# Performance work log

Measured on AMD Instinct MI355X. Metric: run time of the kernel, lower is better.

Reference implementation:

```python
import jax, jax.numpy as jnp
import numpy as np

PC_MIN = jnp.array([0.0, -40.0, -3.0], dtype=jnp.float32)
VS_TOP = jnp.array([0.4, 0.4, 4.0], dtype=jnp.float32)
VS_MED = jnp.array([0.2, 0.2, 2.0], dtype=jnp.float32)
VS_LOW = jnp.array([0.1, 0.1, 1.0], dtype=jnp.float32)
GRID_TOP = (176, 200, 1)
GRID_MED = (352, 400, 2)
GRID_LOW = (704, 800, 4)
EPS = 1e-3
FILL = np.iinfo(np.int32).max


def _bn(x, g, b):
    # training-mode BatchNorm1d over the point/voxel axis (naiveSyncBN1d, eps=1e-3)
    mu = jnp.mean(x, axis=0)
    var = jnp.var(x, axis=0)
    return (x - mu) * jax.lax.rsqrt(var + EPS) * g + b


def _decode(lin, gx, gy, gz):
    x = lin % gx
    r = lin // gx
    y = r % gy
    r = r // gy
    z = r % gz
    b = r // gz
    return b, x, y, z


def _vfe(pts, batch, vs, grid, W1, g1, b1, W2, g2, b2):
    # Dynamic voxelization + DynamicScatterVFE (cluster center + voxel center, 2 layers, scatter-mean).
    N = pts.shape[0]
    gx, gy, gz = grid
    xyz = pts[:, :3]
    coors = jnp.floor((xyz - PC_MIN) / vs).astype(jnp.int32)
    cx = jnp.clip(coors[:, 0], 0, gx - 1)
    cy = jnp.clip(coors[:, 1], 0, gy - 1)
    cz = jnp.clip(coors[:, 2], 0, gz - 1)
    lin = ((batch * gz + cz) * gy + cy) * gx + cx  # linear voxel id incl. batch
    uniq, inv = jnp.unique(lin, return_inverse=True, size=N, fill_value=FILL)
    valid = uniq != FILL
    cnt = jnp.maximum(jax.ops.segment_sum(jnp.ones((N,), pts.dtype), inv, num_segments=N), 1.0)
    seg_mean = lambda v: jax.ops.segment_sum(v, inv, num_segments=N) / cnt[:, None]
    f_cluster = xyz - seg_mean(xyz)[inv]                      # offset from per-voxel point mean
    centers = PC_MIN + (jnp.stack([cx, cy, cz], axis=1).astype(pts.dtype) + 0.5) * vs
    f_center = xyz - centers                                   # offset from voxel center
    feats = jnp.concatenate([pts, f_cluster, f_center], axis=1)  # [N, 10]
    h = jax.nn.relu(_bn(feats @ W1, g1, b1))
    h = jnp.concatenate([h, seg_mean(h)[inv]], axis=1)           # point feat || gathered voxel feat
    h = jax.nn.relu(_bn(h @ W2, g2, b2))
    vox = seg_mean(h)
    return jnp.where(valid[:, None], vox, 0.0), uniq, valid


def _merge(sub_feats, sub_uniq, sub_valid, top_uniq, sub_grid, factor):
    # find_coordinate_indices + scatter_v2(mode='avg'): mean of child voxel feats per parent voxel.
    b, x, y, z = _decode(sub_uniq, *sub_grid)
    gx, gy, gz = GRID_TOP
    parent = ((b * gz + z // factor) * gy + y // factor) * gx + x // factor
    M = top_uniq.shape[0]
    pos = jnp.clip(jnp.searchsorted(top_uniq, parent), 0, M - 1)
    found = sub_valid & (top_uniq[pos] == parent)
    seg = jnp.where(found, pos, M)  # unmatched/padding rows dropped into slot M
    s = jax.ops.segment_sum(sub_feats, seg, num_segments=M + 1)[:M]
    c = jax.ops.segment_sum(found.astype(sub_feats.dtype), seg, num_segments=M + 1)[:M]
    return s / jnp.maximum(c, 1.0)[:, None]


def setup_inputs() -> dict:
    key = jax.random.key(0)
    ks = jax.random.split(key, 12)
    N, B = 262144, 2
    x = jax.random.uniform(ks[0], (N, 1), jnp.float32, 0.0, 70.4)
    y = jax.random.uniform(ks[1], (N, 1), jnp.float32, -40.0, 40.0)
    z = jax.random.uniform(ks[2], (N, 1), jnp.float32, -3.0, 1.0)
    inten = jax.random.uniform(ks[3], (N, 1), jnp.float32)
    bcol = jnp.repeat(jnp.arange(B, dtype=jnp.float32), N // B)[:, None]
    points = jnp.concatenate([bcol, x, y, z, inten], axis=1)
    lin_w = lambda k, i, o: jax.random.normal(k, (i, o), jnp.float32) * (1.0 / np.sqrt(i))
    return dict(
        points=points, batch_size=2,
        W1_top=lin_w(ks[4], 10, 64), g1_top=jnp.ones(64), b1_top=jnp.zeros(64),
        W2_top=lin_w(ks[5], 128, 128), g2_top=jnp.ones(128), b2_top=jnp.zeros(128),
        W1_med=lin_w(ks[6], 10, 32), g1_med=jnp.ones(32), b1_med=jnp.zeros(32),
        W2_med=lin_w(ks[7], 64, 64), g2_med=jnp.ones(64), b2_med=jnp.zeros(64),
        W1_low=lin_w(ks[8], 10, 32), g1_low=jnp.ones(32), b1_low=jnp.zeros(32),
        W2_low=lin_w(ks[9], 64, 64), g2_low=jnp.ones(64), b2_low=jnp.zeros(64),
    )


def reference(points, batch_size, W1_top, g1_top, b1_top, W2_top, g2_top, b2_top,
              W1_med, g1_med, b1_med, W2_med, g2_med, b2_med,
              W1_low, g1_low, b1_low, W2_low, g2_low, b2_low):
    batch = points[:, 0].astype(jnp.int32)
    pts = points[:, 1:]
    vf, top_uniq, top_valid = _vfe(pts, batch, VS_TOP, GRID_TOP, W1_top, g1_top, b1_top, W2_top, g2_top, b2_top)
    mfeat, med_uniq, med_valid = _vfe(pts, batch, VS_MED, GRID_MED, W1_med, g1_med, b1_med, W2_med, g2_med, b2_med)
    lfeat, low_uniq, low_valid = _vfe(pts, batch, VS_LOW, GRID_LOW, W1_low, g1_low, b1_low, W2_low, g2_low, b2_low)
    med_mean = _merge(mfeat, med_uniq, med_valid, top_uniq, GRID_MED, 2)
    low_mean = _merge(lfeat, low_uniq, low_valid, top_uniq, GRID_LOW, 4)
    merged = jnp.where(top_valid[:, None], jnp.concatenate([med_mean, low_mean], axis=1), 0.0)
    b, x, y, z = _decode(top_uniq, *GRID_TOP)
    coors = jnp.where(top_valid[:, None], jnp.stack([b, z, y, x], axis=1), -1)
    return vf, merged, coors
```

## Files before the change

kernel.cpp:

```cpp
#include <hip/hip_runtime.h>
#include <cstdint>
#include <cstddef>

#define NPTS 262144
#define BLK 256
#define TGX 176
#define TGY 200
#define TGZ 1

#define G_TOPC 70400
#define G_MEDC 1126400
#define G_LOWC 4505600

#define SCAN_ITEMS 32
#define SCAN_CHUNK (BLK*SCAN_ITEMS)
#define NB_T 9
#define NB_M 138
#define NB_L 550
#define BO_T 0
#define BO_M 16
#define BO_L 160
#define NBVT (G_TOPC/BLK)
#define NBVM (NPTS/BLK)
#define NBVL (NPTS/BLK)

#define Y2B (NPTS/128)
#define ST1BLKS 256
#define NHT 4400
#define NHM 8192
#define NJT 8800
#define NJM 16384
#define NCL 275

struct SP {
  const float4* srt; const int* jr; const float4* vm;
  const float* W1; const float* W2;
  const float* g1; const float* b1; const float* g2; const float* b2;
  const int* cnt; const int* uniq; const int* woff; const int* U;
  float* segt; float* part1; float* part2;
  float* coef1; float* coef2;
  unsigned short* Y2;
  float* hout;
  int C1; int segstride; int gx, gy, gz; float vx, vy, vz;
};

__device__ __forceinline__ unsigned short f2bf(float v) {
  unsigned u = __float_as_uint(v);
  u += 0x7FFFu + ((u >> 16) & 1u);
  return (unsigned short)(u >> 16);
}
__device__ __forceinline__ float bf2f(unsigned short h) {
  return __uint_as_float((unsigned)h << 16);
}

__device__ __forceinline__ void pcoords(float x, float y, float z,
    float vx, float vy, float vz, int gx, int gy, int gz,
    int& cx, int& cy, int& cz) {
  cx = (int)floorf((x - 0.0f)  / vx);
  cy = (int)floorf((y + 40.0f) / vy);
  cz = (int)floorf((z + 3.0f)  / vz);
  cx = min(max(cx, 0), gx - 1);
  cy = min(max(cy, 0), gy - 1);
  cz = min(max(cz, 0), gz - 1);
}

__device__ __forceinline__ int lin3(float b, float x, float y, float z,
    float vx, float vy, float vz, int gx, int gy, int gz) {
  int cx, cy, cz; pcoords(x, y, z, vx, vy, vz, gx, gy, gz, cx, cy, cz);
  return (((int)b * gz + cz) * gy + cy) * gx + cx;
}

__device__ __forceinline__ void build_f(float4 p, float4 vm,
    float vx, float vy, float vz, int gx, int gy, int gz, float* f) {
  int cx, cy, cz; pcoords(p.x, p.y, p.z, vx, vy, vz, gx, gy, gz, cx, cy, cz);
  f[0] = p.x; f[1] = p.y; f[2] = p.z; f[3] = p.w;
  f[4] = p.x - vm.x;
  f[5] = p.y - vm.y;
  f[6] = p.z - vm.z;
  f[7] = p.x - (0.0f   + (cx + 0.5f)*vx);
  f[8] = p.y - (-40.0f + (cy + 0.5f)*vy);
  f[9] = p.z - (-3.0f  + (cz + 0.5f)*vz);
}

__global__ __launch_bounds__(BLK) void k_count3(const float* __restrict__ pts,
    int* __restrict__ ct, int* __restrict__ cm, int* __restrict__ cl) {
  int i = blockIdx.x * BLK + threadIdx.x;
  if (i >= NPTS) return;
  float b = pts[i*5+0], x = pts[i*5+1], y = pts[i*5+2], z = pts[i*5+3];
  atomicAdd(&ct[lin3(b,x,y,z, 0.4f,0.4f,4.0f, 176,200,1)], 1);
  atomicAdd(&cm[lin3(b,x,y,z, 0.2f,0.2f,2.0f, 352,400,2)], 1);
  atomicAdd(&cl[lin3(b,x,y,z, 0.1f,0.1f,1.0f, 704,800,4)], 1);
}

__global__ __launch_bounds__(BLK) void k_scan1_all(const int* __restrict__ ct,
    const int* __restrict__ cm, const int* __restrict__ cl,
    int2* __restrict__ bsum) {
  int bid = blockIdx.x;
  const int* cnt; int G, bo, cb;
  if (bid < NB_T)            { cnt = ct; G = G_TOPC; bo = BO_T; cb = bid; }
  else if (bid < NB_T+NB_M)  { cnt = cm; G = G_MEDC; bo = BO_M; cb = bid - NB_T; }
  else                       { cnt = cl; G = G_LOWC; bo = BO_L; cb = bid - NB_T - NB_M; }
  int base = cb * SCAN_CHUNK + threadIdx.x * SCAN_ITEMS;
  int so = 0, sp = 0;
  #pragma unroll
  for (int k = 0; k < SCAN_ITEMS; k++) {
    int j = base + k;
    if (j < G) { int c = cnt[j]; if (c > 0) { so++; sp += c; } }
  }
  __shared__ int sho[BLK], shp[BLK];
  sho[threadIdx.x] = so; shp[threadIdx.x] = sp; __syncthreads();
  for (int off = BLK/2; off > 0; off >>= 1) {
    if (threadIdx.x < off) {
      sho[threadIdx.x] += sho[threadIdx.x + off];
      shp[threadIdx.x] += shp[threadIdx.x + off];
    }
    __syncthreads();
  }
  if (threadIdx.x == 0) { int2 v; v.x = sho[0]; v.y = shp[0]; bsum[bo + cb] = v; }
}

__device__ void scan_pass(int2* bsum, int off, int nb, int* U,
                          int* so, int* sp) {
  int t = threadIdx.x;
  int vo = 0, vp = 0;
  if (t < nb) { int2 v = bsum[off + t]; vo = v.x; vp = v.y; }
  so[t] = vo; sp[t] = vp; __syncthreads();
  for (int o = 1; o < 1024; o <<= 1) {
    int ao = (t >= o) ? so[t - o] : 0;
    int ap = (t >= o) ? sp[t - o] : 0;
    __syncthreads();
    so[t] += ao; sp[t] += ap;
    __syncthreads();
  }
  if (t < nb) { int2 e; e.x = so[t] - vo; e.y = sp[t] - vp; bsum[off + t] = e; }
  if (t == 0) *U = so[1023];
  __syncthreads();
}

__global__ __launch_bounds__(1024) void k_scan2_all(int2* __restrict__ bsum,
    int* __restrict__ Ut, int* __restrict__ Um, int* __restrict__ Ul) {
  __shared__ int so[1024], sp[1024];
  scan_pass(bsum, BO_T, NB_T, Ut, so, sp);
  scan_pass(bsum, BO_M, NB_M, Um, so, sp);
  scan_pass(bsum, BO_L, NB_L, Ul, so, sp);
}

__global__ __launch_bounds__(BLK) void k_scan3_all(const int* __restrict__ ct,
    const int* __restrict__ cm, const int* __restrict__ cl,
    const int2* __restrict__ bsum,
    int* __restrict__ rkt, int* __restrict__ rkm, int* __restrict__ rkl,
    int* __restrict__ uqt, int* __restrict__ uqm, int* __restrict__ uql,
    int* __restrict__ wot, int* __restrict__ wom, int* __restrict__ wol) {
  int bid = blockIdx.x;
  const int* cnt; int G, bo, cb; int *rank, *uniq, *woff;
  if (bid < NB_T)           { cnt=ct; G=G_TOPC; bo=BO_T; cb=bid;            rank=rkt; uniq=uqt; woff=wot; }
  else if (bid < NB_T+NB_M) { cnt=cm; G=G_MEDC; bo=BO_M; cb=bid-NB_T;       rank=rkm; uniq=uqm; woff=wom; }
  else                      { cnt=cl; G=G_LOWC; bo=BO_L; cb=bid-NB_T-NB_M;  rank=rkl; uniq=uql; woff=wol; }
  int base = cb * SCAN_CHUNK + threadIdx.x * SCAN_ITEMS;
  int so = 0, sp = 0;
  #pragma unroll
  for (int k = 0; k < SCAN_ITEMS; k++) {
    int j = base + k;
    if (j < G) { int c = cnt[j]; if (c > 0) { so++; sp += c; } }
  }
  __shared__ int sho[BLK], shp[BLK];
  sho[threadIdx.x] = so; shp[threadIdx.x] = sp; __syncthreads();
  for (int off = 1; off < BLK; off <<= 1) {
    int ao = (threadIdx.x >= off) ? sho[threadIdx.x - off] : 0;
    int ap = (threadIdx.x >= off) ? shp[threadIdx.x - off] : 0;
    __syncthreads();
    sho[threadIdx.x] += ao; shp[threadIdx.x] += ap;
    __syncthreads();
  }
  int2 bb = bsum[bo + cb];
  int ro = bb.x + sho[threadIdx.x] - so;
  int po = bb.y + shp[threadIdx.x] - sp;
  for (int k = 0; k < SCAN_ITEMS; k++) {
    int j = base + k;
    if (j < G) {
      int c = cnt[j];
      if (c > 0) { rank[j] = ro; uniq[ro] = j; woff[ro] = po; ro++; po += c; }
    }
  }
}

__global__ __launch_bounds__(BLK) void k_scatter3(const float* __restrict__ pts,
    const int* __restrict__ rkt, int* __restrict__ wot, float4* __restrict__ st, int* __restrict__ jt,
    const int* __restrict__ rkm, int* __restrict__ wom, float4* __restrict__ sm, int* __restrict__ jm,
    const int* __restrict__ rkl, int* __restrict__ wol, float4* __restrict__ sl, int* __restrict__ jl) {
  int i = blockIdx.x * BLK + threadIdx.x;
  if (i >= NPTS) return;
  float b = pts[i*5+0], x = pts[i*5+1], y = pts[i*5+2], z = pts[i*5+3], it = pts[i*5+4];
  float4 p; p.x = x; p.y = y; p.z = z; p.w = it;
  {
    int r = rkt[lin3(b,x,y,z, 0.4f,0.4f,4.0f, 176,200,1)];
    int j = atomicAdd(&wot[r], 1); st[j] = p; jt[j] = r;
  }
  {
    int r = rkm[lin3(b,x,y,z, 0.2f,0.2f,2.0f, 352,400,2)];
    int j = atomicAdd(&wom[r], 1); sm[j] = p; jm[j] = r;
  }
  {
    int r = rkl[lin3(b,x,y,z, 0.1f,0.1f,1.0f, 704,800,4)];
    int j = atomicAdd(&wol[r], 1); sl[j] = p; jl[j] = r;
  }
}

__global__ __launch_bounds__(BLK) void k_vox13(
    const float4* __restrict__ st, const int* __restrict__ uqt, const int* __restrict__ ct,
    const int* __restrict__ wot, const int* __restrict__ Ut, float4* __restrict__ vt,
    const float4* __restrict__ sm, const int* __restrict__ uqm, const int* __restrict__ cm,
    const int* __restrict__ wom, const int* __restrict__ Um, float4* __restrict__ vm,
    const float4* __restrict__ sl, const int* __restrict__ uql, const int* __restrict__ cl,
    const int* __restrict__ wol, const int* __restrict__ Ul, float4* __restrict__ vl) {
  int bid = blockIdx.x;
  const float4* srt; const int *uniq, *cnt, *woff, *Up; float4* vmean; int r;
  if (bid < NBVT)           { r = bid*BLK + threadIdx.x;           srt=st; uniq=uqt; cnt=ct; woff=wot; Up=Ut; vmean=vt; }
  else if (bid < NBVT+NBVM) { r = (bid-NBVT)*BLK + threadIdx.x;    srt=sm; uniq=uqm; cnt=cm; woff=wom; Up=Um; vmean=vm; }
  else                      { r = (bid-NBVT-NBVM)*BLK + threadIdx.x; srt=sl; uniq=uql; cnt=cl; woff=wol; Up=Ul; vmean=vl; }
  if (r >= *Up) return;
  int lin = uniq[r];
  int len = cnt[lin];
  int base = woff[r] - len;
  float sx = 0.f, sy = 0.f, sz = 0.f;
  for (int k = 0; k < len; k++) {
    float4 p = srt[base + k];
    sx += p.x; sy += p.y; sz += p.z;
  }
  float il = 1.0f / (float)len;
  float4 o; o.x = sx*il; o.y = sy*il; o.z = sz*il; o.w = il;
  vmean[r] = o;
}

__global__ __launch_bounds__(BLK) void k_stats1_all(SP a, SP b, SP c) {
  int s = blockIdx.x >> 8;
  int blk = blockIdx.x & 255;
  SP sp = (s == 0) ? a : ((s == 1) ? b : c);
  const int C1 = sp.C1;
  __shared__ float w[640];
  __shared__ float wsum[4][64], wsq[4][64];
  for (int t = threadIdx.x; t < 10*C1; t += BLK) w[t] = sp.W1[t];
  __syncthreads();
  float f[4][10];
  #pragma unroll
  for (int k = 0; k < 4; k++) {
    int i = blk*1024 + k*BLK + threadIdx.x;
    float4 p = sp.srt[i];
    float4 vmn = sp.vm[sp.jr[i]];
    build_f(p, vmn, sp.vx, sp.vy, sp.vz, sp.gx, sp.gy, sp.gz, f[k]);
  }
  int wv = threadIdx.x >> 6;
  int lane = threadIdx.x & 63;
  for (int o = 0; o < C1; o += 4) {
    float sacc[4] = {0,0,0,0}, qacc[4] = {0,0,0,0};
    #pragma unroll
    for (int k = 0; k < 4; k++) {
      float a0=0.f, a1=0.f, a2=0.f, a3=0.f;
      #pragma unroll
      for (int d = 0; d < 10; d++) {
        float fv = f[k][d];
        const float* wr = &w[d*C1 + o];
        a0 = fmaf(fv, wr[0], a0); a1 = fmaf(fv, wr[1], a1);
        a2 = fmaf(fv, wr[2], a2); a3 = fmaf(fv, wr[3], a3);
      }
      sacc[0] += a0; sacc[1] += a1; sacc[2] += a2; sacc[3] += a3;
      qacc[0] += a0*a0; qacc[1] += a1*a1; qacc[2] += a2*a2; qacc[3] += a3*a3;
    }
    #pragma unroll
    for (int m = 1; m < 64; m <<= 1) {
      #pragma unroll
      for (int e = 0; e < 4; e++) {
        sacc[e] += __shfl_xor(sacc[e], m);
        qacc[e] += __shfl_xor(qacc[e], m);
      }
    }
    if (lane == 0) {
      #pragma unroll
      for (int e = 0; e < 4; e++) { wsum[wv][o+e] = sacc[e]; wsq[wv][o+e] = qacc[e]; }
    }
  }
  __syncthreads();
  if (threadIdx.x < C1) {
    int ch = threadIdx.x;
    float sv = wsum[0][ch] + wsum[1][ch] + wsum[2][ch] + wsum[3][ch];
    float qv = wsq[0][ch] + wsq[1][ch] + wsq[2][ch] + wsq[3][ch];
    sp.part1[(size_t)blk*2*C1 + ch]      = sv;
    sp.part1[(size_t)blk*2*C1 + C1 + ch] = qv;
  }
}

__device__ __forceinline__ void partcoef_body(const float* part, int NB, int C,
    int ch, const float* g, const float* b, float* coef) {
  float s = 0.f, q = 0.f;
  for (int bk = threadIdx.x; bk < NB; bk += BLK) {
    s += part[(size_t)bk*2*C + ch];
    q += part[(size_t)bk*2*C + C + ch];
  }
  __shared__ float ss[BLK], sq[BLK];
  ss[threadIdx.x] = s; sq[threadIdx.x] = q; __syncthreads();
  for (int off = BLK/2; off > 0; off >>= 1) {
    if (threadIdx.x < off) {
      ss[threadIdx.x] += ss[threadIdx.x + off];
      sq[threadIdx.x] += sq[threadIdx.x + off];
    }
    __syncthreads();
  }
  if (threadIdx.x == 0) {
    float mu  = ss[0] * (1.0f / NPTS);
    float var = sq[0] * (1.0f / NPTS) - mu*mu;
    float sc  = g[ch] * (1.0f / sqrtf(var + 1e-3f));
    coef[ch]     = sc;
    coef[C + ch] = fmaf(-mu, sc, b[ch]);
  }
}

__global__ __launch_bounds__(BLK) void k_partcoef1_all(SP a, SP b, SP c) {
  int bid = blockIdx.x; SP sp; int ch;
  if (bid < 64)      { sp = a; ch = bid; }
  else if (bid < 96) { sp = b; ch = bid - 64; }
  else               { sp = c; ch = bid - 96; }
  if (ch >= sp.C1) return;
  partcoef_body(sp.part1, ST1BLKS, sp.C1, ch, sp.g1, sp.b1, sp.coef1);
}

__global__ __launch_bounds__(BLK) void k_partcoef2_all(SP a, SP b, SP c) {
  int bid = blockIdx.x; SP sp; int ch;
  if (bid < 128)      { sp = a; ch = bid; }
  else if (bid < 192) { sp = b; ch = bid - 128; }
  else                { sp = c; ch = bid - 192; }
  if (ch >= 2*sp.C1) return;
  partcoef_body(sp.part2, Y2B, 2*sp.C1, ch, sp.g2, sp.b2, sp.coef2);
}

__global__ __launch_bounds__(BLK) void k_hsegT_all(SP a, SP b, SP c) {
  int bid = blockIdx.x; SP sp; int rb;
  if (bid < NHT)           { sp = a; rb = bid; }
  else if (bid < NHT+NHM)  { sp = b; rb = bid - NHT; }
  else                     { sp = c; rb = bid - NHT - NHM; }
  const int C1 = sp.C1;
  const int qsh = (C1 == 64) ? 4 : 3;
  __shared__ float w[640];
  __shared__ float sc[64], sb[64];
  for (int t = threadIdx.x; t < 10*C1; t += BLK) w[t] = sp.W1[t];
  for (int t = threadIdx.x; t < C1; t += BLK) { sc[t] = sp.coef1[t]; sb[t] = sp.coef1[C1 + t]; }
  __syncthreads();
  int tid = rb * BLK + threadIdx.x;
  int r = tid >> qsh;
  int q = tid & ((1 << qsh) - 1);
  if (r >= *sp.U) return;
  int lin = sp.uniq[r];
  int len = sp.cnt[lin];
  int base = sp.woff[r] - len;
  float4 vmn = sp.vm[r];
  int c0 = q * 4;
  float s0 = sc[c0+0], s1 = sc[c0+1], s2 = sc[c0+2], s3 = sc[c0+3];
  float o0 = sb[c0+0], o1 = sb[c0+1], o2 = sb[c0+2], o3 = sb[c0+3];
  float a0=0.f, a1=0.f, a2=0.f, a3=0.f;
  for (int k = 0; k < len; k++) {
    float4 p = sp.srt[base + k];
    float f[10];
    build_f(p, vmn, sp.vx, sp.vy, sp.vz, sp.gx, sp.gy, sp.gz, f);
    float y0=0.f, y1=0.f, y2=0.f, y3=0.f;
    #pragma unroll
    for (int d = 0; d < 10; d++) {
      float fv = f[d];
      const float* wr = &w[d*C1 + c0];
      y0 = fmaf(fv, wr[0], y0); y1 = fmaf(fv, wr[1], y1);
      y2 = fmaf(fv, wr[2], y2); y3 = fmaf(fv, wr[3], y3);
    }
    a0 += fmaxf(fmaf(y0, s0, o0), 0.f);
    a1 += fmaxf(fmaf(y1, s1, o1), 0.f);
    a2 += fmaxf(fmaf(y2, s2, o2), 0.f);
    a3 += fmaxf(fmaf(y3, s3, o3), 0.f);
  }
  float il = 1.0f / (float)len;
  sp.segt[(size_t)(c0+0)*sp.segstride + r] = a0*il;
  sp.segt[(size_t)(c0+1)*sp.segstride + r] = a1*il;
  sp.segt[(size_t)(c0+2)*sp.segstride + r] = a2*il;
  sp.segt[(size_t)(c0+3)*sp.segstride + r] = a3*il;
}

#define FMA4(ACC, AV, BV) { (ACC).x = fmaf((AV), (BV).x, (ACC).x); \
  (ACC).y = fmaf((AV), (BV).y, (ACC).y); \
  (ACC).z = fmaf((AV), (BV).z, (ACC).z); \
  (ACC).w = fmaf((AV), (BV).w, (ACC).w); }

template<int C1>
__device__ __forceinline__ void y2t_body(const SP& sp, int blk,
    float* At, float* Bp) {
  constexpr int C2  = 2*C1;
  constexpr int K   = 2*C1;
  constexpr int MT  = 128;
  constexpr int KC  = 32;
  constexpr int NKC = K / KC;
  constexpr int NP  = C2 / 64;
  const int tid  = threadIdx.x;
  const int base = blk * MT;

  const int jst = tid & 127;
  const int qst = tid >> 7;
  int    jr_s = sp.jr[base + jst];
  float4 p_s  = sp.srt[base + jst];
  float4 vm_s = sp.vm[jr_s];
  float fs[10];
  build_f(p_s, vm_s, sp.vx, sp.vy, sp.vz, sp.gx, sp.gy, sp.gz, fs);

  const int w      = tid >> 6;
  const int lane   = tid & 63;
  const int colg   = lane & 15;
  const int rowsub = lane >> 4;
  const int rowg   = w*4 + rowsub;
  const int arow   = rowg*8;

  float4 acc[NP][8];
  #pragma unroll
  for (int p = 0; p < NP; p++)
    #pragma unroll
    for (int rr = 0; rr < 8; rr++) acc[p][rr] = {0.f, 0.f, 0.f, 0.f};

  #pragma unroll
  for (int kc = 0; kc < NKC; kc++) {
    if (kc) __syncthreads();
    if (kc*KC < C1) {
      #pragma unroll
      for (int m = 0; m < 4; m++) {
        int qq = qst + 2*m;
        int c0 = kc*KC + qq*4;
        float y0=0.f, y1=0.f, y2=0.f, y3=0.f;
        #pragma unroll
        for (int d = 0; d < 10; d++) {
          float fv = fs[d];
          const float* wr = &sp.W1[d*C1 + c0];
          y0 = fmaf(fv, wr[0], y0); y1 = fmaf(fv, wr[1], y1);
          y2 = fmaf(fv, wr[2], y2); y3 = fmaf(fv, wr[3], y3);
        }
        At[(qq*4+0)*MT + jst] = fmaxf(fmaf(y0, sp.coef1[c0+0], sp.coef1[C1+c0+0]), 0.f);
        At[(qq*4+1)*MT + jst] = fmaxf(fmaf(y1, sp.coef1[c0+1], sp.coef1[C1+c0+1]), 0.f);
        At[(qq*4+2)*MT + jst] = fmaxf(fmaf(y2, sp.coef1[c0+2], sp.coef1[C1+c0+2]), 0.f);
        At[(qq*4+3)*MT + jst] = fmaxf(fmaf(y3, sp.coef1[c0+3], sp.coef1[C1+c0+3]), 0.f);
      }
    } else {
      #pragma unroll
      for (int m = 0; m < 16; m++) {
        int k = qst + 2*m;
        int segch = kc*KC + k - C1;
        At[k*MT + jst] = sp.segt[(size_t)segch*sp.segstride + jr_s];
      }
    }
    constexpr int BQ = KC*C2/4;
    for (int it = tid; it < BQ; it += BLK) {
      int k  = it / (C2/4);
      int c4 = it % (C2/4);
      *(float4*)&Bp[k*C2 + c4*4] =
          *(const float4*)&sp.W2[(size_t)(kc*KC + k)*C2 + c4*4];
    }
    __syncthreads();
    #pragma unroll 8
    for (int k = 0; k < KC; k++) {
      float4 a0 = *(const float4*)&At[k*MT + arow];
      float4 a1 = *(const float4*)&At[k*MT + arow + 4];
      #pragma unroll
      for (int p = 0; p < NP; p++) {
        float4 bv = *(const float4*)&Bp[k*C2 + p*64 + colg*4];
        FMA4(acc[p][0], a0.x, bv); FMA4(acc[p][1], a0.y, bv);
        FMA4(acc[p][2], a0.z, bv); FMA4(acc[p][3], a0.w, bv);
        FMA4(acc[p][4], a1.x, bv); FMA4(acc[p][5], a1.y, bv);
        FMA4(acc[p][6], a1.z, bv); FMA4(acc[p][7], a1.w, bv);
      }
    }
  }

  #pragma unroll
  for (int p = 0; p < NP; p++)
    #pragma unroll
    for (int rr = 0; rr < 8; rr++) {
      float4 v = acc[p][rr];
      ushort4 h; h.x = f2bf(v.x); h.y = f2bf(v.y); h.z = f2bf(v.z); h.w = f2bf(v.w);
      *(ushort4*)&sp.Y2[(size_t)(base + arow + rr)*C2 + p*64 + colg*4] = h;
    }

  __syncthreads();
  float* red = At;
  #pragma unroll
  for (int p = 0; p < NP; p++) {
    #pragma unroll
    for (int e = 0; e < 4; e++) {
      float sv = 0.f, qv = 0.f;
      #pragma unroll
      for (int rr = 0; rr < 8; rr++) {
        float v = (&acc[p][rr].x)[e];
        sv += v; qv += v*v;
      }
      red[rowg*C2 + p*64 + colg*4 + e]        = sv;
      red[(16 + rowg)*C2 + p*64 + colg*4 + e] = qv;
    }
  }
  __syncthreads();
  if (tid < C2) {
    float sv = 0.f, qv = 0.f;
    #pragma unroll 4
    for (int i = 0; i < 16; i++) {
      sv += red[i*C2 + tid];
      qv += red[(16 + i)*C2 + tid];
    }
    sp.part2[(size_t)blk*2*C2 + tid]      = sv;
    sp.part2[(size_t)blk*2*C2 + C2 + tid] = qv;
  }
}

__global__ __launch_bounds__(BLK) void k_y2t_all(SP a, SP b, SP c) {
  __shared__ float At[32*128];
  __shared__ float Bp[32*128];
  int bid = blockIdx.x;
  if (bid < Y2B)        y2t_body<64>(a, bid, At, Bp);
  else if (bid < 2*Y2B) y2t_body<32>(b, bid - Y2B, At, Bp);
  else                  y2t_body<32>(c, bid - 2*Y2B, At, Bp);
}

__global__ __launch_bounds__(BLK) void k_hseg2_all(SP a, SP b, SP c) {
  int bid = blockIdx.x; SP sp; int rb;
  if (bid < NJT)           { sp = a; rb = bid; }
  else if (bid < NJT+NJM)  { sp = b; rb = bid - NJT; }
  else                     { sp = c; rb = bid - NJT - NJM; }
  const int C = 2*sp.C1;
  const int qsh = (C == 128) ? 5 : 4;
  __shared__ float sc[128], sb[128];
  for (int t = threadIdx.x; t < C; t += BLK) { sc[t] = sp.coef2[t]; sb[t] = sp.coef2[C + t]; }
  __syncthreads();
  int tid = rb * BLK + threadIdx.x;
  int r = tid >> qsh;
  int q = tid & ((1 << qsh) - 1);
  if (r >= *sp.U) return;
  int lin = sp.uniq[r];
  int len = sp.cnt[lin];
  int base = sp.woff[r] - len;
  int c0 = q * 4;
  float s0 = sc[c0+0], s1 = sc[c0+1], s2 = sc[c0+2], s3 = sc[c0+3];
  float o0 = sb[c0+0], o1 = sb[c0+1], o2 = sb[c0+2], o3 = sb[c0+3];
  float a0=0.f, a1=0.f, a2=0.f, a3=0.f;
  const unsigned short* Yh = sp.Y2;
  for (int k = 0; k < len; k++) {
    ushort4 hv = *(const ushort4*)&Yh[(size_t)(base + k)*C + c0];
    a0 += fmaxf(fmaf(bf2f(hv.x), s0, o0), 0.f);
    a1 += fmaxf(fmaf(bf2f(hv.y), s1, o1), 0.f);
    a2 += fmaxf(fmaf(bf2f(hv.z), s2, o2), 0.f);
    a3 += fmaxf(fmaf(bf2f(hv.w), s3, o3), 0.f);
  }
  float il = 1.0f / (float)len;
  float4 o = {a0*il, a1*il, a2*il, a3*il};
  *(float4*)&sp.hout[(size_t)r*C + c0] = o;
}

__global__ __launch_bounds__(BLK) void k_clist_all(const int* __restrict__ tuniq,
    const int* __restrict__ Utp,
    const int* __restrict__ cnt_m, const int* __restrict__ rank_m,
    int* __restrict__ clist_m, int* __restrict__ mcnt_m,
    const int* __restrict__ cnt_l, const int* __restrict__ rank_l,
    int* __restrict__ clist_l, int* __restrict__ mcnt_l) {
  int bid = blockIdx.x;
  const int *scnt, *srank; int *clist, *mcnt;
  int gx, gy, gz, f, rb;
  if (bid < NCL) { scnt=cnt_m; srank=rank_m; clist=clist_m; mcnt=mcnt_m;
                   gx=352; gy=400; gz=2; f=2; rb=bid; }
  else           { scnt=cnt_l; srank=rank_l; clist=clist_l; mcnt=mcnt_l;
                   gx=704; gy=800; gz=4; f=4; rb=bid-NCL; }
  int r = rb * BLK + threadIdx.x;
  if (r >= *Utp) return;
  int lin = tuniq[r];
  int x = lin % TGX; int t = lin / TGX;
  int y = t % TGY;   int b = t / TGY;
  int m = 0;
  for (int cz = 0; cz < gz; cz++)
    for (int yy = y*f; yy < y*f + f; yy++)
      for (int xx = x*f; xx < x*f + f; xx++) {
        int cl = ((b*gz + cz)*gy + yy)*gx + xx;
        if (scnt[cl] > 0) clist[(size_t)r*64 + (m++)] = srank[cl];
      }
  mcnt[r] = m;
}

__global__ __launch_bounds__(BLK) void k_merge2_all(
    const float* __restrict__ vox_m, const int* __restrict__ clist_m,
    const int* __restrict__ mcnt_m, float* __restrict__ maccm,
    const float* __restrict__ vox_l, const int* __restrict__ clist_l,
    const int* __restrict__ mcnt_l, float* __restrict__ maccl,
    const int* __restrict__ Utp) {
  int bid = blockIdx.x;
  const float* vox; const int *clist, *mcnt; float* dest; int rb;
  if (bid < NHT) { vox=vox_m; clist=clist_m; mcnt=mcnt_m; dest=maccm; rb=bid; }
  else           { vox=vox_l; clist=clist_l; mcnt=mcnt_l; dest=maccl; rb=bid-NHT; }
  int idx = rb * BLK + threadIdx.x;
  int r = idx >> 4;
  int q = idx & 15;
  if (r >= *Utp) return;
  int m = mcnt[r];
  float a0=0.f, a1=0.f, a2=0.f, a3=0.f;
  for (int t = 0; t < m; t++) {
    int cr = clist[(size_t)r*64 + t];
    float4 v = *(const float4*)&vox[(size_t)cr*64 + q*4];
    a0 += v.x; a1 += v.y; a2 += v.z; a3 += v.w;
  }
  float inv = 1.0f / (float)max(m, 1);
  float4 o = {a0*inv, a1*inv, a2*inv, a3*inv};
  *(float4*)&dest[(size_t)r*64 + q*4] = o;
}

__global__ __launch_bounds__(BLK) void k_fin_all(const int* __restrict__ uniq,
    const int* __restrict__ Up, const float* __restrict__ maccm,
    const float* __restrict__ maccl, float* __restrict__ vf,
    float* __restrict__ mg, float* __restrict__ coors) {
  int idx = blockIdx.x * BLK + threadIdx.x;
  int r = idx >> 5;
  int q = idx & 31;
  if (r >= NPTS) return;
  int U = *Up;
  float4 v = {0.f, 0.f, 0.f, 0.f};
  if (r < U)
    v = (q < 16) ? *(const float4*)&maccm[(size_t)r*64 + q*4]
                 : *(const float4*)&maccl[(size_t)r*64 + (q-16)*4];
  *(float4*)&mg[(size_t)r*128 + q*4] = v;
  if (r >= U) {
    float4 z = {0.f, 0.f, 0.f, 0.f};
    *(float4*)&vf[(size_t)r*128 + q*4] = z;
  }
  if (q == 0) {
    float4 co;
    if (r < U) {
      int lin = uniq[r];
      int x = lin % TGX; int t = lin / TGX;
      int y = t % TGY;   t /= TGY;
      int z = t % TGZ;   int b = t / TGZ;
      co.x = (float)b; co.y = (float)z; co.z = (float)y; co.w = (float)x;
    } else {
      co.x = -1.f; co.y = -1.f; co.z = -1.f; co.w = -1.f;
    }
    *(float4*)&coors[(size_t)r*4] = co;
  }
}

extern "C" void kernel_launch(void* const* d_in, const int* in_sizes, int n_in,
                              void* d_out, int out_size, void* d_ws, size_t ws_size,
                              hipStream_t stream) {
  const float* pts = (const float*)d_in[0];

  float* out = (float*)d_out;
  float* vf = out;
  float* mg = out + (size_t)NPTS * 128;
  float* co = out + (size_t)NPTS * 256;

  char* w = (char*)d_ws;
  size_t off = 0;
  auto alloc = [&](size_t bytes) -> void* {
    void* p = w + off;
    off = (off + bytes + 1023) & ~(size_t)1023;
    return p;
  };
  int*    cnt_t   = (int*)alloc(((size_t)G_TOPC + G_MEDC + G_LOWC) * 4);
  int*    cnt_m   = cnt_t + G_TOPC;
  int*    cnt_l   = cnt_t + G_TOPC + G_MEDC;
  int*    rank_t  = (int*)alloc((size_t)G_TOPC * 4);
  int*    rank_m  = (int*)alloc((size_t)G_MEDC * 4);
  int*    rank_l  = (int*)alloc((size_t)G_LOWC * 4);
  int*    uniq_t  = (int*)alloc((size_t)G_TOPC * 4);
  int*    uniq_m  = (int*)alloc((size_t)NPTS * 4);
  int*    uniq_l  = (int*)alloc((size_t)NPTS * 4);
  int*    woff_t  = (int*)alloc((size_t)G_TOPC * 4);
  int*    woff_m  = (int*)alloc((size_t)NPTS * 4);
  int*    woff_l  = (int*)alloc((size_t)NPTS * 4);
  float4* srt_t   = (float4*)alloc((size_t)NPTS * 16);
  float4* srt_m   = (float4*)alloc((size_t)NPTS * 16);
  float4* srt_l   = (float4*)alloc((size_t)NPTS * 16);
  int*    jr_t    = (int*)alloc((size_t)NPTS * 4);
  int*    jr_m    = (int*)alloc((size_t)NPTS * 4);
  int*    jr_l    = (int*)alloc((size_t)NPTS * 4);
  float4* vm_t    = (float4*)alloc((size_t)G_TOPC * 16);
  float4* vm_m    = (float4*)alloc((size_t)NPTS * 16);
  float4* vm_l    = (float4*)alloc((size_t)NPTS * 16);
  float*  segt_t  = (float*)alloc((size_t)G_TOPC * 64 * 4);
  float*  segt_m  = (float*)alloc((size_t)NPTS * 32 * 4);
  float*  segt_l  = (float*)alloc((size_t)NPTS * 32 * 4);
  float*  vox_m   = (float*)alloc((size_t)NPTS * 64 * 4);
  float*  vox_l   = (float*)alloc((size_t)NPTS * 64 * 4);
  unsigned short* Y2h_t = (unsigned short*)alloc((size_t)NPTS * 128 * 2);
  unsigned short* Y2h_m = (unsigned short*)alloc((size_t)NPTS * 64 * 2);
  unsigned short* Y2h_l = (unsigned short*)alloc((size_t)NPTS * 64 * 2);
  int*    clist_m = (int*)alloc((size_t)G_TOPC * 64 * 4);
  int*    clist_l = (int*)alloc((size_t)G_TOPC * 64 * 4);
  int*    mcnt_m  = (int*)alloc((size_t)G_TOPC * 4);
  int*    mcnt_l  = (int*)alloc((size_t)G_TOPC * 4);
  float*  maccm   = (float*)alloc((size_t)G_TOPC * 64 * 4);
  float*  maccl   = (float*)alloc((size_t)G_TOPC * 64 * 4);
  float*  part1_t = (float*)alloc((size_t)ST1BLKS * 128 * 4);
  float*  part1_m = (float*)alloc((size_t)ST1BLKS * 64 * 4);
  float*  part1_l = (float*)alloc((size_t)ST1BLKS * 64 * 4);
  float*  part2_t = (float*)alloc((size_t)Y2B * 256 * 4);
  float*  part2_m = (float*)alloc((size_t)Y2B * 128 * 4);
  float*  part2_l = (float*)alloc((size_t)Y2B * 128 * 4);
  float*  coef    = (float*)alloc(6 * 256 * 4);
  int2*   bsum    = (int2*)alloc(1024 * 8);
  int*    Ut      = (int*)alloc(64);
  int*    Um      = (int*)alloc(64);
  int*    Ul      = (int*)alloc(64);
  (void)in_sizes; (void)n_in; (void)out_size; (void)ws_size;

  auto mkSP = [&](int scaleIdx) -> SP {
    SP s{};
    if (scaleIdx == 0) {
      s.srt = srt_t; s.jr = jr_t; s.vm = vm_t;
      s.W1 = (const float*)d_in[2];  s.g1 = (const float*)d_in[3];
      s.b1 = (const float*)d_in[4];  s.W2 = (const float*)d_in[5];
      s.g2 = (const float*)d_in[6];  s.b2 = (const float*)d_in[7];
      s.cnt = cnt_t; s.uniq = uniq_t; s.woff = woff_t; s.U = Ut;
      s.segt = segt_t; s.part1 = part1_t; s.part2 = part2_t;
      s.coef1 = coef + 0*256; s.coef2 = coef + 1*256;
      s.Y2 = Y2h_t; s.hout = vf;
      s.C1 = 64; s.segstride = G_TOPC;
      s.gx = 176; s.gy = 200; s.gz = 1; s.vx = 0.4f; s.vy = 0.4f; s.vz = 4.0f;
    } else if (scaleIdx == 1) {
      s.srt = srt_m; s.jr = jr_m; s.vm = vm_m;
      s.W1 = (const float*)d_in[8];  s.g1 = (const float*)d_in[9];
      s.b1 = (const float*)d_in[10]; s.W2 = (const float*)d_in[11];
      s.g2 = (const float*)d_in[12]; s.b2 = (const float*)d_in[13];
      s.cnt = cnt_m; s.uniq = uniq_m; s.woff = woff_m; s.U = Um;
      s.segt = segt_m; s.part1 = part1_m; s.part2 = part2_m;
      s.coef1 = coef + 2*256; s.coef2 = coef + 3*256;
      s.Y2 = Y2h_m; s.hout = vox_m;
      s.C1 = 32; s.segstride = NPTS;
      s.gx = 352; s.gy = 400; s.gz = 2; s.vx = 0.2f; s.vy = 0.2f; s.vz = 2.0f;
    } else {
      s.srt = srt_l; s.jr = jr_l; s.vm = vm_l;
      s.W1 = (const float*)d_in[14]; s.g1 = (const float*)d_in[15];
      s.b1 = (const float*)d_in[16]; s.W2 = (const float*)d_in[17];
      s.g2 = (const float*)d_in[18]; s.b2 = (const float*)d_in[19];
      s.cnt = cnt_l; s.uniq = uniq_l; s.woff = woff_l; s.U = Ul;
      s.segt = segt_l; s.part1 = part1_l; s.part2 = part2_l;
      s.coef1 = coef + 4*256; s.coef2 = coef + 5*256;
      s.Y2 = Y2h_l; s.hout = vox_l;
      s.C1 = 32; s.segstride = NPTS;
      s.gx = 704; s.gy = 800; s.gz = 4; s.vx = 0.1f; s.vy = 0.1f; s.vz = 1.0f;
    }
    return s;
  };
  SP spT = mkSP(0), spM = mkSP(1), spL = mkSP(2);

  (void)hipMemsetAsync(cnt_t, 0, ((size_t)G_TOPC + G_MEDC + G_LOWC) * 4, stream);
  k_count3<<<NPTS/BLK, BLK, 0, stream>>>(pts, cnt_t, cnt_m, cnt_l);
  k_scan1_all<<<NB_T + NB_M + NB_L, BLK, 0, stream>>>(cnt_t, cnt_m, cnt_l, bsum);
  k_scan2_all<<<1, 1024, 0, stream>>>(bsum, Ut, Um, Ul);
  k_scan3_all<<<NB_T + NB_M + NB_L, BLK, 0, stream>>>(cnt_t, cnt_m, cnt_l, bsum,
      rank_t, rank_m, rank_l, uniq_t, uniq_m, uniq_l, woff_t, woff_m, woff_l);
  k_clist_all<<<2*NCL, BLK, 0, stream>>>(uniq_t, Ut,
      cnt_m, rank_m, clist_m, mcnt_m, cnt_l, rank_l, clist_l, mcnt_l);
  k_scatter3<<<NPTS/BLK, BLK, 0, stream>>>(pts,
      rank_t, woff_t, srt_t, jr_t,
      rank_m, woff_m, srt_m, jr_m,
      rank_l, woff_l, srt_l, jr_l);
  k_vox13<<<NBVT + NBVM + NBVL, BLK, 0, stream>>>(
      srt_t, uniq_t, cnt_t, woff_t, Ut, vm_t,
      srt_m, uniq_m, cnt_m, woff_m, Um, vm_m,
      srt_l, uniq_l, cnt_l, woff_l, Ul, vm_l);

  k_stats1_all<<<3*ST1BLKS, BLK, 0, stream>>>(spT, spM, spL);
  k_partcoef1_all<<<128, BLK, 0, stream>>>(spT, spM, spL);
  k_hsegT_all<<<NHT + 2*NHM, BLK, 0, stream>>>(spT, spM, spL);
  k_y2t_all<<<3*Y2B, BLK, 0, stream>>>(spT, spM, spL);
  k_partcoef2_all<<<256, BLK, 0, stream>>>(spT, spM, spL);
  k_hseg2_all<<<NJT + 2*NJM, BLK, 0, stream>>>(spT, spM, spL);

  k_merge2_all<<<2*NHT, BLK, 0, stream>>>(vox_m, clist_m, mcnt_m, maccm,
      vox_l, clist_l, mcnt_l, maccl, Ut);
  k_fin_all<<<(NPTS*32)/BLK, BLK, 0, stream>>>(uniq_t, Ut, maccm, maccl,
      vf, mg, co);
}
```

Measured before the change: 728.6 us.

## Compute second VFE layer GEMM with bf16 MFMA instead of FP32 FMAs

```diff
diff --git a/kernel.cpp b/kernel.cpp
--- a/kernel.cpp
+++ b/kernel.cpp
@@ -24,13 +24,16 @@
 #define NBVM (NPTS/BLK)
 #define NBVL (NPTS/BLK)
 
-#define Y2B (NPTS/128)
+#define Y2B2 (NPTS/64)
 #define ST1BLKS 256
 #define NHT 4400
 #define NHM 8192
 #define NJT 8800
 #define NJM 16384
 #define NCL 275
+
+typedef __attribute__((ext_vector_type(8))) short bf16x8;
+typedef __attribute__((ext_vector_type(4))) float f32x4;
 
 struct SP {
   const float4* srt; const int* jr; const float4* vm;
@@ -329,7 +332,7 @@
   else if (bid < 192) { sp = b; ch = bid - 128; }
   else                { sp = c; ch = bid - 192; }
   if (ch >= 2*sp.C1) return;
-  partcoef_body(sp.part2, Y2B, 2*sp.C1, ch, sp.g2, sp.b2, sp.coef2);
+  partcoef_body(sp.part2, Y2B2, 2*sp.C1, ch, sp.g2, sp.b2, sp.coef2);
 }
 
 __global__ __launch_bounds__(BLK) void k_hsegT_all(SP a, SP b, SP c) {
@@ -380,120 +383,102 @@
   sp.segt[(size_t)(c0+3)*sp.segstride + r] = a3*il;
 }
 
-#define FMA4(ACC, AV, BV) { (ACC).x = fmaf((AV), (BV).x, (ACC).x); \
-  (ACC).y = fmaf((AV), (BV).y, (ACC).y); \
-  (ACC).z = fmaf((AV), (BV).z, (ACC).z); \
-  (ACC).w = fmaf((AV), (BV).w, (ACC).w); }
+__global__ __launch_bounds__(BLK) void k_packB_all(
+    const float* __restrict__ W2t_, unsigned short* __restrict__ Bt,
+    const float* __restrict__ W2m_, unsigned short* __restrict__ Bm,
+    const float* __restrict__ W2l_, unsigned short* __restrict__ Bl) {
+  int bid = blockIdx.x;
+  const float* W2; unsigned short* Bp; int C2, idx;
+  if (bid < 64)      { W2 = W2t_; Bp = Bt; C2 = 128; idx = bid*BLK + threadIdx.x; }
+  else if (bid < 80) { W2 = W2m_; Bp = Bm; C2 = 64;  idx = (bid-64)*BLK + threadIdx.x; }
+  else               { W2 = W2l_; Bp = Bl; C2 = 64;  idx = (bid-80)*BLK + threadIdx.x; }
+  if (idx >= C2*C2) return;
+  int NCF = C2/16;
+  int per_kb = NCF*512;
+  int kb = idx / per_kb, rem = idx % per_kb;
+  int cf = rem / 512, r2 = rem % 512;
+  int lane = r2 >> 3, j = r2 & 7;
+  int k = kb*32 + (lane >> 4)*8 + j;
+  int col = cf*16 + (lane & 15);
+  Bp[idx] = f2bf(W2[(size_t)k*C2 + col]);
+}
 
 template<int C1>
-__device__ __forceinline__ void y2t_body(const SP& sp, int blk,
-    float* At, float* Bp) {
+__device__ __forceinline__ void y2m_body(const SP& sp,
+    const unsigned short* __restrict__ Bpk, int blk, unsigned short* Alds) {
+  constexpr int K   = 2*C1;
   constexpr int C2  = 2*C1;
-  constexpr int K   = 2*C1;
-  constexpr int MT  = 128;
-  constexpr int KC  = 32;
-  constexpr int NKC = K / KC;
-  constexpr int NP  = C2 / 64;
+  constexpr int MT  = 64;
+  constexpr int NKB = K / 32;
+  constexpr int NCF = C2 / 16;
+  constexpr int RB  = K * 2;
   const int tid  = threadIdx.x;
   const int base = blk * MT;
 
-  const int jst = tid & 127;
-  const int qst = tid >> 7;
-  int    jr_s = sp.jr[base + jst];
-  float4 p_s  = sp.srt[base + jst];
-  float4 vm_s = sp.vm[jr_s];
-  float fs[10];
-  build_f(p_s, vm_s, sp.vx, sp.vy, sp.vz, sp.gx, sp.gy, sp.gz, fs);
-
-  const int w      = tid >> 6;
-  const int lane   = tid & 63;
-  const int colg   = lane & 15;
-  const int rowsub = lane >> 4;
-  const int rowg   = w*4 + rowsub;
-  const int arow   = rowg*8;
-
-  float4 acc[NP][8];
-  #pragma unroll
-  for (int p = 0; p < NP; p++)
+  {
+    const int jst = tid & 63;
+    const int qst = tid >> 6;
+    int jr = sp.jr[base + jst];
+    float4 p = sp.srt[base + jst];
+    float4 vmn = sp.vm[jr];
+    float fs[10];
+    build_f(p, vmn, sp.vx, sp.vy, sp.vz, sp.gx, sp.gy, sp.gz, fs);
+    const int k_lo = qst * (K/4);
     #pragma unroll
-    for (int rr = 0; rr < 8; rr++) acc[p][rr] = {0.f, 0.f, 0.f, 0.f};
-
-  #pragma unroll
-  for (int kc = 0; kc < NKC; kc++) {
-    if (kc) __syncthreads();
-    if (kc*KC < C1) {
-      #pragma unroll
-      for (int m = 0; m < 4; m++) {
-        int qq = qst + 2*m;
-        int c0 = kc*KC + qq*4;
-        float y0=0.f, y1=0.f, y2=0.f, y3=0.f;
+    for (int kk = 0; kk < K/8; kk++) {
+      int k0 = k_lo + kk*2;
+      float v0, v1;
+      if (k0 < C1) {
+        float y0 = 0.f, y1v = 0.f;
         #pragma unroll
         for (int d = 0; d < 10; d++) {
-          float fv = fs[d];
-          const float* wr = &sp.W1[d*C1 + c0];
-          y0 = fmaf(fv, wr[0], y0); y1 = fmaf(fv, wr[1], y1);
-          y2 = fmaf(fv, wr[2], y2); y3 = fmaf(fv, wr[3], y3);
+          y0  = fmaf(fs[d], sp.W1[d*C1 + k0],     y0);
+          y1v = fmaf(fs[d], sp.W1[d*C1 + k0 + 1], y1v);
         }
-        At[(qq*4+0)*MT + jst] = fmaxf(fmaf(y0, sp.coef1[c0+0], sp.coef1[C1+c0+0]), 0.f);
-        At[(qq*4+1)*MT + jst] = fmaxf(fmaf(y1, sp.coef1[c0+1], sp.coef1[C1+c0+1]), 0.f);
-        At[(qq*4+2)*MT + jst] = fmaxf(fmaf(y2, sp.coef1[c0+2], sp.coef1[C1+c0+2]), 0.f);
-        At[(qq*4+3)*MT + jst] = fmaxf(fmaf(y3, sp.coef1[c0+3], sp.coef1[C1+c0+3]), 0.f);
+        v0 = fmaxf(fmaf(y0,  sp.coef1[k0],   sp.coef1[C1 + k0]),   0.f);
+        v1 = fmaxf(fmaf(y1v, sp.coef1[k0+1], sp.coef1[C1 + k0+1]), 0.f);
+      } else {
+        v0 = sp.segt[(size_t)(k0     - C1)*sp.segstride + jr];
+        v1 = sp.segt[(size_t)(k0 + 1 - C1)*sp.segstride + jr];
       }
-    } else {
-      #pragma unroll
-      for (int m = 0; m < 16; m++) {
-        int k = qst + 2*m;
-        int segch = kc*KC + k - C1;
-        At[k*MT + jst] = sp.segt[(size_t)segch*sp.segstride + jr_s];
-      }
-    }
-    constexpr int BQ = KC*C2/4;
-    for (int it = tid; it < BQ; it += BLK) {
-      int k  = it / (C2/4);
-      int c4 = it % (C2/4);
-      *(float4*)&Bp[k*C2 + c4*4] =
-          *(const float4*)&sp.W2[(size_t)(kc*KC + k)*C2 + c4*4];
-    }
-    __syncthreads();
-    #pragma unroll 8
-    for (int k = 0; k < KC; k++) {
-      float4 a0 = *(const float4*)&At[k*MT + arow];
-      float4 a1 = *(const float4*)&At[k*MT + arow + 4];
-      #pragma unroll
-      for (int p = 0; p < NP; p++) {
-        float4 bv = *(const float4*)&Bp[k*C2 + p*64 + colg*4];
-        FMA4(acc[p][0], a0.x, bv); FMA4(acc[p][1], a0.y, bv);
-        FMA4(acc[p][2], a0.z, bv); FMA4(acc[p][3], a0.w, bv);
-        FMA4(acc[p][4], a1.x, bv); FMA4(acc[p][5], a1.y, bv);
-        FMA4(acc[p][6], a1.z, bv); FMA4(acc[p][7], a1.w, bv);
-      }
-    }
-  }
-
+      unsigned u = (unsigned)f2bf(v0) | ((unsigned)f2bf(v1) << 16);
+      int g  = k0 >> 3;
+      int gp = g ^ (jst & 7);
+      *(unsigned*)((char*)Alds + (size_t)jst*RB + gp*16 + (k0 & 7)*2) = u;
+    }
+  }
+  __syncthreads();
+
+  const int w    = tid >> 6;
+  const int l    = tid & 63;
+  const int rowf = l & 15;
+  const int kg   = l >> 4;
+  const int row  = w*16 + rowf;
+  f32x4 acc[NCF];
   #pragma unroll
-  for (int p = 0; p < NP; p++)
+  for (int cf = 0; cf < NCF; cf++) acc[cf] = (f32x4){0.f, 0.f, 0.f, 0.f};
+  #pragma unroll
+  for (int kb = 0; kb < NKB; kb++) {
+    int g  = kb*4 + kg;
+    int gp = g ^ (row & 7);
+    bf16x8 a = *(const bf16x8*)((const char*)Alds + (size_t)row*RB + gp*16);
+    const bf16x8* bfr = (const bf16x8*)Bpk + (size_t)(kb*NCF)*64 + l;
     #pragma unroll
-    for (int rr = 0; rr < 8; rr++) {
-      float4 v = acc[p][rr];
-      ushort4 h; h.x = f2bf(v.x); h.y = f2bf(v.y); h.z = f2bf(v.z); h.w = f2bf(v.w);
-      *(ushort4*)&sp.Y2[(size_t)(base + arow + rr)*C2 + p*64 + colg*4] = h;
-    }
-
-  __syncthreads();
-  float* red = At;
+    for (int cf = 0; cf < NCF; cf++) {
+      bf16x8 b = bfr[cf*64];
+      acc[cf] = __builtin_amdgcn_mfma_f32_16x16x32_bf16(a, b, acc[cf], 0, 0, 0);
+    }
+  }
+
+  __syncthreads();
+  float* red = (float*)Alds;
   #pragma unroll
-  for (int p = 0; p < NP; p++) {
-    #pragma unroll
-    for (int e = 0; e < 4; e++) {
-      float sv = 0.f, qv = 0.f;
-      #pragma unroll
-      for (int rr = 0; rr < 8; rr++) {
-        float v = (&acc[p][rr].x)[e];
-        sv += v; qv += v*v;
-      }
-      red[rowg*C2 + p*64 + colg*4 + e]        = sv;
-      red[(16 + rowg)*C2 + p*64 + colg*4 + e] = qv;
-    }
+  for (int cf = 0; cf < NCF; cf++) {
+    f32x4 v = acc[cf];
+    float sv = v.x + v.y + v.z + v.w;
+    float qv = v.x*v.x + v.y*v.y + v.z*v.z + v.w*v.w;
+    red[(w*4 + kg)*C2 + cf*16 + rowf]        = sv;
+    red[(16 + w*4 + kg)*C2 + cf*16 + rowf]   = qv;
   }
   __syncthreads();
   if (tid < C2) {
@@ -506,15 +491,34 @@
     sp.part2[(size_t)blk*2*C2 + tid]      = sv;
     sp.part2[(size_t)blk*2*C2 + C2 + tid] = qv;
   }
-}
-
-__global__ __launch_bounds__(BLK) void k_y2t_all(SP a, SP b, SP c) {
-  __shared__ float At[32*128];
-  __shared__ float Bp[32*128];
+  __syncthreads();
+
+  unsigned short* D = Alds;
+  #pragma unroll
+  for (int cf = 0; cf < NCF; cf++) {
+    #pragma unroll
+    for (int rg = 0; rg < 4; rg++) {
+      int rr = w*16 + kg*4 + rg;
+      D[rr*C2 + cf*16 + rowf] = f2bf(acc[cf][rg]);
+    }
+  }
+  __syncthreads();
+  for (int it = tid; it < MT*C2/8; it += BLK) {
+    int r = (it*8) / C2;
+    int c = (it*8) % C2;
+    uint4 v = *(const uint4*)&D[it*8];
+    *(uint4*)&sp.Y2[(size_t)(base + r)*C2 + c] = v;
+  }
+}
+
+__global__ __launch_bounds__(BLK) void k_y2m_all(SP a, SP b, SP c,
+    const unsigned short* __restrict__ Bt, const unsigned short* __restrict__ Bm,
+    const unsigned short* __restrict__ Bl) {
+  __shared__ unsigned short Alds[64*128];
   int bid = blockIdx.x;
-  if (bid < Y2B)        y2t_body<64>(a, bid, At, Bp);
-  else if (bid < 2*Y2B) y2t_body<32>(b, bid - Y2B, At, Bp);
-  else                  y2t_body<32>(c, bid - 2*Y2B, At, Bp);
+  if (bid < Y2B2)        y2m_body<64>(a, Bt, bid, Alds);
+  else if (bid < 2*Y2B2) y2m_body<32>(b, Bm, bid - Y2B2, Alds);
+  else                   y2m_body<32>(c, Bl, bid - 2*Y2B2, Alds);
 }
 
 __global__ __launch_bounds__(BLK) void k_hseg2_all(SP a, SP b, SP c) {
@@ -684,6 +688,9 @@
   unsigned short* Y2h_t = (unsigned short*)alloc((size_t)NPTS * 128 * 2);
   unsigned short* Y2h_m = (unsigned short*)alloc((size_t)NPTS * 64 * 2);
   unsigned short* Y2h_l = (unsigned short*)alloc((size_t)NPTS * 64 * 2);
+  unsigned short* Bpk_t = (unsigned short*)alloc(16384 * 2);
+  unsigned short* Bpk_m = (unsigned short*)alloc(4096 * 2);
+  unsigned short* Bpk_l = (unsigned short*)alloc(4096 * 2);
   int*    clist_m = (int*)alloc((size_t)G_TOPC * 64 * 4);
   int*    clist_l = (int*)alloc((size_t)G_TOPC * 64 * 4);
   int*    mcnt_m  = (int*)alloc((size_t)G_TOPC * 4);
@@ -693,9 +700,9 @@
   float*  part1_t = (float*)alloc((size_t)ST1BLKS * 128 * 4);
   float*  part1_m = (float*)alloc((size_t)ST1BLKS * 64 * 4);
   float*  part1_l = (float*)alloc((size_t)ST1BLKS * 64 * 4);
-  float*  part2_t = (float*)alloc((size_t)Y2B * 256 * 4);
-  float*  part2_m = (float*)alloc((size_t)Y2B * 128 * 4);
-  float*  part2_l = (float*)alloc((size_t)Y2B * 128 * 4);
+  float*  part2_t = (float*)alloc((size_t)Y2B2 * 256 * 4);
+  float*  part2_m = (float*)alloc((size_t)Y2B2 * 128 * 4);
+  float*  part2_l = (float*)alloc((size_t)Y2B2 * 128 * 4);
   float*  coef    = (float*)alloc(6 * 256 * 4);
   int2*   bsum    = (int2*)alloc(1024 * 8);
   int*    Ut      = (int*)alloc(64);
@@ -743,6 +750,9 @@
   };
   SP spT = mkSP(0), spM = mkSP(1), spL = mkSP(2);
 
+  k_packB_all<<<96, BLK, 0, stream>>>((const float*)d_in[5], Bpk_t,
+      (const float*)d_in[11], Bpk_m, (const float*)d_in[17], Bpk_l);
+
   (void)hipMemsetAsync(cnt_t, 0, ((size_t)G_TOPC + G_MEDC + G_LOWC) * 4, stream);
   k_count3<<<NPTS/BLK, BLK, 0, stream>>>(pts, cnt_t, cnt_m, cnt_l);
   k_scan1_all<<<NB_T + NB_M + NB_L, BLK, 0, stream>>>(cnt_t, cnt_m, cnt_l, bsum);
@@ -763,7 +773,7 @@
   k_stats1_all<<<3*ST1BLKS, BLK, 0, stream>>>(spT, spM, spL);
   k_partcoef1_all<<<128, BLK, 0, stream>>>(spT, spM, spL);
   k_hsegT_all<<<NHT + 2*NHM, BLK, 0, stream>>>(spT, spM, spL);
-  k_y2t_all<<<3*Y2B, BLK, 0, stream>>>(spT, spM, spL);
+  k_y2m_all<<<3*Y2B2, BLK, 0, stream>>>(spT, spM, spL, Bpk_t, Bpk_m, Bpk_l);
   k_partcoef2_all<<<256, BLK, 0, stream>>>(spT, spM, spL);
   k_hseg2_all<<<NJT + 2*NJM, BLK, 0, stream>>>(spT, spM, spL);
 
```

Measured after the change: 692.1 us. 1.05x faster.
